# Kernel tuning notes

Measured on AMD Instinct MI355X. Metric: run time of the kernel, lower is better.

## Reference

```python
import jax, jax.numpy as jnp
import numpy as np

N_NODES = 50000


def _graphconv(h, W, b, src, dst, norm_src, norm_dst, activation):
    # DGL GraphConv, norm='both': scale by out-degree^{-1/2} on src side,
    # aggregate (copy_u + sum), scale by in-degree^{-1/2} on dst side.
    in_f, out_f = W.shape
    h = h * norm_src[:, None]
    if in_f > out_f:
        # mult W first to reduce message size (matches DGL branch)
        h = h @ W
        h = jax.ops.segment_sum(h[src], dst, num_segments=N_NODES)
    else:
        h = jax.ops.segment_sum(h[src], dst, num_segments=N_NODES)
        h = h @ W
    h = h * norm_dst[:, None] + b
    if activation:
        h = jax.nn.relu(h)
    return h


def setup_inputs() -> dict:
    key = jax.random.key(0)
    ks = jax.random.split(key, 10)
    N, E = N_NODES, 800000
    in_feats, n_hidden, n_classes = 256, 128, 64
    features = jax.random.normal(ks[0], (N, in_feats), dtype=jnp.float32)
    src = jax.random.randint(ks[1], (E,), 0, N, dtype=jnp.int32)
    dst = jax.random.randint(ks[2], (E,), 0, N, dtype=jnp.int32)
    def glorot(k, shape):
        lim = float(np.sqrt(6.0 / (shape[0] + shape[1])))
        return jax.random.uniform(k, shape, jnp.float32, -lim, lim)
    return {
        "features": features,
        "W1": glorot(ks[3], (in_feats, n_hidden)), "b1": jnp.zeros((n_hidden,), jnp.float32),
        "W2": glorot(ks[4], (n_hidden, n_hidden)), "b2": jnp.zeros((n_hidden,), jnp.float32),
        "W3": glorot(ks[5], (n_hidden, n_classes)), "b3": jnp.zeros((n_classes,), jnp.float32),
        "src": src, "dst": dst,
    }


def reference(features, W1, b1, W2, b2, W3, b3, src, dst):
    ones = jnp.ones(src.shape, jnp.float32)
    deg_out = jax.ops.segment_sum(ones, src, num_segments=N_NODES)
    deg_in = jax.ops.segment_sum(ones, dst, num_segments=N_NODES)
    norm_src = jax.lax.rsqrt(jnp.maximum(deg_out, 1.0))
    norm_dst = jax.lax.rsqrt(jnp.maximum(deg_in, 1.0))
    h = features
    # dropout in eval mode (identity) for deterministic baseline
    h = _graphconv(h, W1, b1, src, dst, norm_src, norm_dst, activation=True)
    h = _graphconv(h, W2, b2, src, dst, norm_src, norm_dst, activation=True)
    h = _graphconv(h, W3, b3, src, dst, norm_src, norm_dst, activation=False)
    return h
```

## Files before the change

### kernel.cpp

```cpp
#include <hip/hip_runtime.h>
#include <math.h>


typedef _Float16 half8 __attribute__((ext_vector_type(8)));
typedef float floatx4 __attribute__((ext_vector_type(4)));

#define TILE 1024
#define BCAP 8192
#define PKW  64
#define EPT  4

__global__ __launch_bounds__(256) void bin_edges(
    const int* __restrict__ src, const int* __restrict__ dst, int E, int NB,
    int* __restrict__ gcurD, int* __restrict__ gcurS,
    ushort2* __restrict__ binD, unsigned short* __restrict__ binS)
{
    __shared__ int lcntD[256], loffD[256], curD[256], lbaseD[256];
    __shared__ int lcntS[256], loffS[256], curS[256], lbaseS[256];
    __shared__ int wtot[4];
    __shared__ ushort2 stageD[TILE];
    __shared__ unsigned short stageS[TILE];

    const int tid = threadIdx.x, lane = tid & 63, wave = tid >> 6;
    const int tile0 = blockIdx.x * TILE;
    const int tn = min(TILE, E - tile0);

    lcntD[tid] = 0;
    lcntS[tid] = 0;
    __syncthreads();

    unsigned short es[EPT], ed[EPT];
    unsigned char ebD[EPT], ebS[EPT];
    int nl = 0;
    for (int i = tid; i < tn; i += 256) {
        int s = src[tile0 + i], d = dst[tile0 + i];
        es[nl] = (unsigned short)s; ed[nl] = (unsigned short)d;
        ebD[nl] = (unsigned char)(d >> 8);
        ebS[nl] = (unsigned char)(s >> 8);
        nl++;
        atomicAdd(&lcntD[d >> 8], 1);
        atomicAdd(&lcntS[s >> 8], 1);
    }
    __syncthreads();

    {
        int v = lcntD[tid], x = v;
#pragma unroll
        for (int o = 1; o < 64; o <<= 1) {
            int t = __shfl_up(x, o, 64);
            if (lane >= o) x += t;
        }
        if (lane == 63) wtot[wave] = x;
        __syncthreads();
        if (tid == 0) {
            int a = 0;
#pragma unroll
            for (int w = 0; w < 4; w++) { int t = wtot[w]; wtot[w] = a; a += t; }
        }
        __syncthreads();
        int excl = x - v + wtot[wave];
        loffD[tid] = excl;
        curD[tid]  = excl;
    }
    __syncthreads();
    {
        int v = lcntS[tid], x = v;
#pragma unroll
        for (int o = 1; o < 64; o <<= 1) {
            int t = __shfl_up(x, o, 64);
            if (lane >= o) x += t;
        }
        if (lane == 63) wtot[wave] = x;
        __syncthreads();
        if (tid == 0) {
            int a = 0;
#pragma unroll
            for (int w = 0; w < 4; w++) { int t = wtot[w]; wtot[w] = a; a += t; }
        }
        __syncthreads();
        int excl = x - v + wtot[wave];
        loffS[tid] = excl;
        curS[tid]  = excl;
    }
    __syncthreads();

    for (int j = 0; j < nl; j++) {
        int pD = atomicAdd(&curD[ebD[j]], 1);
        ushort2 u; u.x = es[j]; u.y = ed[j];
        stageD[pD] = u;
        int pS = atomicAdd(&curS[ebS[j]], 1);
        stageS[pS] = es[j];
    }
    if (tid < NB) {
        if (lcntD[tid] > 0) lbaseD[tid] = atomicAdd(&gcurD[tid], lcntD[tid]);
        if (lcntS[tid] > 0) lbaseS[tid] = atomicAdd(&gcurS[tid], lcntS[tid]);
    }
    __syncthreads();

    for (int i = tid; i < tn; i += 256) {
        {
            int lo = 0, hi = NB - 1;
            while (lo < hi) {
                int mid = (lo + hi + 1) >> 1;
                if (loffD[mid] <= i) lo = mid; else hi = mid - 1;
            }
            int gi = lbaseD[lo] + (i - loffD[lo]);
            if (gi < BCAP)
                binD[(size_t)lo * BCAP + gi] = stageD[i];
        }
        {
            int lo = 0, hi = NB - 1;
            while (lo < hi) {
                int mid = (lo + hi + 1) >> 1;
                if (loffS[mid] <= i) lo = mid; else hi = mid - 1;
            }
            int gi = lbaseS[lo] + (i - loffS[lo]);
            if (gi < BCAP)
                binS[(size_t)lo * BCAP + gi] = stageS[i];
        }
    }
}

__global__ __launch_bounds__(256) void lists_counts(
    const ushort2* __restrict__ binD, const int* __restrict__ gcurD,
    const unsigned short* __restrict__ binS, const int* __restrict__ gcurS,
    unsigned short* __restrict__ packed, int* __restrict__ cntI,
    int* __restrict__ cntO, int N, unsigned short padv)
{
    __shared__ unsigned short stage[256 * PKW];
    __shared__ int lcnt[256];
    __shared__ int h[256];
    const int tid = threadIdx.x;
    const int b = blockIdx.x;
    const int node0 = b << 8;

    lcnt[tid] = 0;
    h[tid] = 0;
    for (int i = tid; i < 256 * PKW; i += 256)
        stage[i] = padv;
    __syncthreads();

    const int nD = min(gcurD[b], BCAP);
    const ushort2* ebD = binD + (size_t)b * BCAP;
    for (int i = tid; i < nD; i += 256) {
        ushort2 e = ebD[i];
        int ld = (int)e.y - node0;
        int p = atomicAdd(&lcnt[ld], 1);
        if (p < PKW) stage[ld * PKW + p] = e.x;
    }
    const int nS = min(gcurS[b], BCAP);
    const unsigned short* ebS = binS + (size_t)b * BCAP;
    for (int i = tid; i < nS; i += 256)
        atomicAdd(&h[(int)ebS[i] - node0], 1);
    __syncthreads();

    int node = node0 + tid;
    if (node < N) {
        cntI[node] = min(lcnt[tid], PKW);
        cntO[node] = h[tid];
    }
    const int wave = tid >> 6, lane = tid & 63;
    for (int ld = wave; ld < 256; ld += 4) {
        int nd = node0 + ld;
        if (nd < N)
            packed[(size_t)nd * PKW + lane] = stage[ld * PKW + lane];
    }
}

__global__ __launch_bounds__(256) void wprep(
    const float* __restrict__ W1, const float* __restrict__ W2,
    const float* __restrict__ W3, _Float16* __restrict__ WT1,
    _Float16* __restrict__ WT2, _Float16* __restrict__ WT3,
    int* __restrict__ gcur, _Float16* __restrict__ z0,
    _Float16* __restrict__ z1)
{
    int i = blockIdx.x * 256 + threadIdx.x;
    if (i < 512) gcur[i] = 0;
    else if (i < 640) z0[i - 512] = (_Float16)0.f;
    else if (i < 768) z1[i - 640] = (_Float16)0.f;
    if (i < 256 * 128) {
        int k = i / 128, n = i - k * 128;
        WT1[(size_t)n * 256 + k] = (_Float16)W1[i];
    } else if (i < 256 * 128 + 128 * 128) {
        int r = i - 256 * 128;
        int k = r / 128, n = r - k * 128;
        WT2[(size_t)n * 128 + k] = (_Float16)W2[r];
    } else if (i < 256 * 128 + 128 * 128 + 128 * 64) {
        int r = i - 256 * 128 - 128 * 128;
        int k = r / 64, n = r - k * 64;
        WT3[(size_t)n * 128 + k] = (_Float16)W3[r];
    }
}

template<int K, int NC, bool A_FP32>
__global__ __launch_bounds__(256) void gemm_mfma(
    const void* __restrict__ A_, const _Float16* __restrict__ WT,
    const int* __restrict__ cnt_rs,
    const int* __restrict__ cnt_nd, const float* __restrict__ bias,
    int do_relu, const int* __restrict__ cnt_ns,
    _Float16* __restrict__ C, int M)
{
    constexpr int NT  = NC / 16;
    constexpr int KC  = 128;
    constexpr int LDW = KC + 8;
    __shared__ _Float16 Bs[NC * LDW];

    const int tid  = threadIdx.x;
    const int wave = tid >> 6;
    const int lane = tid & 63;
    const int quad = lane >> 4;
    const int l16  = lane & 15;

    const int row_base = blockIdx.x * 128 + wave * 32;
    const int ar0 = min(row_base + l16, M - 1);
    const int ar1 = min(row_base + 16 + l16, M - 1);

    floatx4 acc[2][NT];
#pragma unroll
    for (int m = 0; m < 2; m++)
#pragma unroll
        for (int t = 0; t < NT; t++)
            acc[m][t] = (floatx4){0.f, 0.f, 0.f, 0.f};

    float rs0 = 1.0f, rs1 = 1.0f;
    if (A_FP32 && cnt_rs) {
        rs0 = rsqrtf(fmaxf((float)cnt_rs[ar0], 1.0f));
        rs1 = rsqrtf(fmaxf((float)cnt_rs[ar1], 1.0f));
    }

    const float*    Af = (const float*)A_;
    const _Float16* Ah = (const _Float16*)A_;

    for (int kc = 0; kc < K; kc += KC) {
#pragma unroll
        for (int s = tid; s < NC * (KC / 8); s += 256) {
            int row  = s >> 4;
            int col8 = s & 15;
            half8 v = *(const half8*)&WT[(size_t)row * K + kc + col8 * 8];
            *(half8*)&Bs[row * LDW + col8 * 8] = v;
        }
        __syncthreads();
#pragma unroll
        for (int k0 = 0; k0 < KC; k0 += 32) {
            half8 a0, a1;
            if (A_FP32) {
                const float* p0 = &Af[(size_t)ar0 * K + kc + k0 + quad * 8];
                const float* p1 = &Af[(size_t)ar1 * K + kc + k0 + quad * 8];
                float4 f0 = *(const float4*)p0;
                float4 f1 = *(const float4*)(p0 + 4);
                float4 g0 = *(const float4*)p1;
                float4 g1 = *(const float4*)(p1 + 4);
                a0[0] = (_Float16)(f0.x * rs0); a0[1] = (_Float16)(f0.y * rs0);
                a0[2] = (_Float16)(f0.z * rs0); a0[3] = (_Float16)(f0.w * rs0);
                a0[4] = (_Float16)(f1.x * rs0); a0[5] = (_Float16)(f1.y * rs0);
                a0[6] = (_Float16)(f1.z * rs0); a0[7] = (_Float16)(f1.w * rs0);
                a1[0] = (_Float16)(g0.x * rs1); a1[1] = (_Float16)(g0.y * rs1);
                a1[2] = (_Float16)(g0.z * rs1); a1[3] = (_Float16)(g0.w * rs1);
                a1[4] = (_Float16)(g1.x * rs1); a1[5] = (_Float16)(g1.y * rs1);
                a1[6] = (_Float16)(g1.z * rs1); a1[7] = (_Float16)(g1.w * rs1);
            } else {
                a0 = *(const half8*)&Ah[(size_t)ar0 * K + kc + k0 + quad * 8];
                a1 = *(const half8*)&Ah[(size_t)ar1 * K + kc + k0 + quad * 8];
            }
#pragma unroll
            for (int t = 0; t < NT; t++) {
                half8 b = *(const half8*)&Bs[(t * 16 + l16) * LDW + k0 + quad * 8];
                acc[0][t] = __builtin_amdgcn_mfma_f32_16x16x32_f16(a0, b, acc[0][t], 0, 0, 0);
                acc[1][t] = __builtin_amdgcn_mfma_f32_16x16x32_f16(a1, b, acc[1][t], 0, 0, 0);
            }
        }
        __syncthreads();
    }

#pragma unroll
    for (int m = 0; m < 2; m++) {
#pragma unroll
        for (int t = 0; t < NT; t++) {
            int col = t * 16 + l16;
            float bv = bias ? bias[col] : 0.f;
#pragma unroll
            for (int r = 0; r < 4; r++) {
                int row_o = row_base + m * 16 + quad * 4 + r;
                if (row_o < M) {
                    float v = acc[m][t][r];
                    if (cnt_nd) v *= rsqrtf(fmaxf((float)cnt_nd[row_o], 1.0f));
                    v += bv;
                    if (do_relu) v = fmaxf(v, 0.f);
                    if (cnt_ns) v *= rsqrtf(fmaxf((float)cnt_ns[row_o], 1.0f));
                    C[(size_t)row_o * NC + col] = (_Float16)v;
                }
            }
        }
    }
}

__global__ __launch_bounds__(256) void gather128(
    const _Float16* __restrict__ msg, const int* __restrict__ cntI,
    const int* __restrict__ cntO, const unsigned short* __restrict__ packed,
    const float* __restrict__ bias, int do_relu, int use_nd, int use_ns,
    _Float16* __restrict__ out, int N)
{
    int node = (blockIdx.x * 256 + threadIdx.x) >> 6;
    if (node >= N) return;
    int lane = threadIdx.x & 63;
    int grp = lane >> 4, l16 = lane & 15;

    int len = cntI[node];
    const unsigned short* bl = packed + (size_t)node * PKW;
    const half8* mp = (const half8*)msg;

    float a[8];
#pragma unroll
    for (int h = 0; h < 8; h++) a[h] = 0.f;

    int iters = (len + 31) >> 5;
    if (iters < 1) iters = 1;
    for (int it = 0; it < iters; it++) {
        int j = it * 32 + grp;
        int s0 = bl[j],      s1 = bl[j + 4],  s2 = bl[j + 8],  s3 = bl[j + 12];
        int s4 = bl[j + 16], s5 = bl[j + 20], s6 = bl[j + 24], s7 = bl[j + 28];
        half8 v0 = mp[(size_t)s0 * 16 + l16];
        half8 v1 = mp[(size_t)s1 * 16 + l16];
        half8 v2 = mp[(size_t)s2 * 16 + l16];
        half8 v3 = mp[(size_t)s3 * 16 + l16];
        half8 v4 = mp[(size_t)s4 * 16 + l16];
        half8 v5 = mp[(size_t)s5 * 16 + l16];
        half8 v6 = mp[(size_t)s6 * 16 + l16];
        half8 v7 = mp[(size_t)s7 * 16 + l16];
#pragma unroll
        for (int h = 0; h < 8; h++)
            a[h] += (((float)v0[h] + (float)v1[h]) + ((float)v2[h] + (float)v3[h]))
                  + (((float)v4[h] + (float)v5[h]) + ((float)v6[h] + (float)v7[h]));
    }
#pragma unroll
    for (int h = 0; h < 8; h++) {
        a[h] += __shfl_xor(a[h], 16);
        a[h] += __shfl_xor(a[h], 32);
    }

    if (grp == 0) {
        float sc = use_nd ? rsqrtf(fmaxf((float)len, 1.0f)) : 1.0f;
        float pp = use_ns ? rsqrtf(fmaxf((float)cntO[node], 1.0f)) : 1.0f;
        half8 rv;
#pragma unroll
        for (int h = 0; h < 8; h++) {
            float bv = bias ? bias[l16 * 8 + h] : 0.f;
            float r = a[h] * sc + bv;
            if (do_relu) r = fmaxf(r, 0.f);
            rv[h] = (_Float16)(r * pp);
        }
        ((half8*)out)[(size_t)node * 16 + l16] = rv;
    }
}

__global__ __launch_bounds__(256) void gather64(
    const _Float16* __restrict__ msg, const int* __restrict__ cntI,
    const unsigned short* __restrict__ packed, const float* __restrict__ bias,
    float* __restrict__ out, int N)
{
    int node = (blockIdx.x * 256 + threadIdx.x) >> 6;
    if (node >= N) return;
    int lane = threadIdx.x & 63;
    int grp = lane >> 3, l8 = lane & 7;

    int len = cntI[node];
    const unsigned short* bl = packed + (size_t)node * PKW;
    const half8* mp = (const half8*)msg;

    float a[8];
#pragma unroll
    for (int h = 0; h < 8; h++) a[h] = 0.f;

    int iters = (len + 31) >> 5;
    if (iters < 1) iters = 1;
    for (int it = 0; it < iters; it++) {
        int j = it * 32 + grp;
        int s0 = bl[j], s1 = bl[j + 8], s2 = bl[j + 16], s3 = bl[j + 24];
        half8 v0 = mp[(size_t)s0 * 8 + l8];
        half8 v1 = mp[(size_t)s1 * 8 + l8];
        half8 v2 = mp[(size_t)s2 * 8 + l8];
        half8 v3 = mp[(size_t)s3 * 8 + l8];
#pragma unroll
        for (int h = 0; h < 8; h++)
            a[h] += ((float)v0[h] + (float)v1[h]) + ((float)v2[h] + (float)v3[h]);
    }
#pragma unroll
    for (int h = 0; h < 8; h++) {
        a[h] += __shfl_xor(a[h], 8);
        a[h] += __shfl_xor(a[h], 16);
        a[h] += __shfl_xor(a[h], 32);
    }

    if (grp == 0) {
        float sc = rsqrtf(fmaxf((float)len, 1.0f));
        float4 r0, r1;
        r0.x = a[0] * sc + bias[l8 * 8 + 0];
        r0.y = a[1] * sc + bias[l8 * 8 + 1];
        r0.z = a[2] * sc + bias[l8 * 8 + 2];
        r0.w = a[3] * sc + bias[l8 * 8 + 3];
        r1.x = a[4] * sc + bias[l8 * 8 + 4];
        r1.y = a[5] * sc + bias[l8 * 8 + 5];
        r1.z = a[6] * sc + bias[l8 * 8 + 6];
        r1.w = a[7] * sc + bias[l8 * 8 + 7];
        float4* op = (float4*)&out[(size_t)node * 64 + l8 * 8];
        op[0] = r0;
        op[1] = r1;
    }
}

extern "C" void kernel_launch(void* const* d_in, const int* in_sizes, int n_in,
                              void* d_out, int out_size, void* d_ws, size_t ws_size,
                              hipStream_t stream)
{
    const float* X  = (const float*)d_in[0];
    const float* W1 = (const float*)d_in[1];
    const float* b1 = (const float*)d_in[2];
    const float* W2 = (const float*)d_in[3];
    const float* b2 = (const float*)d_in[4];
    const float* W3 = (const float*)d_in[5];
    const float* b3 = (const float*)d_in[6];
    const int*   src = (const int*)d_in[7];
    const int*   dst = (const int*)d_in[8];

    const int N = in_sizes[0] / 256;
    const int E = in_sizes[7];
    const int NB = (N + 255) >> 8;

    char* base = (char*)d_ws;
    size_t cur = 0;
    auto alloc = [&](size_t bytes) -> void* {
        void* p = base + cur;
        cur += (bytes + 255) & ~(size_t)255;
        return p;
    };
    int* gcur2 = (int*)alloc((size_t)2 * 256 * 4);
    int* gcurD = gcur2;
    int* gcurS = gcur2 + 256;
    ushort2*        binD   = (ushort2*)alloc((size_t)NB * BCAP * 4);
    unsigned short* binS   = (unsigned short*)alloc((size_t)NB * BCAP * 2);
    unsigned short* packed = (unsigned short*)alloc((size_t)N * PKW * 2);
    int* cntO = (int*)alloc((size_t)N * 4);
    int* cntI = (int*)alloc((size_t)N * 4);
    _Float16* Bh0 = (_Float16*)alloc(((size_t)N + 1) * 128 * 2);
    _Float16* Bh1 = (_Float16*)alloc(((size_t)N + 1) * 128 * 2);
    _Float16* WT1 = (_Float16*)alloc((size_t)256 * 128 * 2);
    _Float16* WT2 = (_Float16*)alloc((size_t)128 * 128 * 2);
    _Float16* WT3 = (_Float16*)alloc((size_t)128 * 64 * 2);

    const int tblk = (E + TILE - 1) / TILE;
    const int gblk = (N + 127) / 128;
    const int wblk = (N + 3) / 4;

    wprep<<<(256*128 + 128*128 + 128*64 + 255) / 256, 256, 0, stream>>>(
        W1, W2, W3, WT1, WT2, WT3,
        gcur2, Bh0 + (size_t)N * 128, Bh1 + (size_t)N * 128);
    bin_edges<<<tblk, 256, 0, stream>>>(src, dst, E, NB, gcurD, gcurS, binD, binS);
    lists_counts<<<NB, 256, 0, stream>>>(binD, gcurD, binS, gcurS,
                                         packed, cntI, cntO, N,
                                         (unsigned short)N);

    gemm_mfma<256, 128, true><<<gblk, 256, 0, stream>>>(
        X, WT1, cntO, nullptr, nullptr, 0, nullptr, Bh0, N);
    gather128<<<wblk, 256, 0, stream>>>(
        Bh0, cntI, cntO, packed, b1, 1, 1, 1, Bh1, N);

    gather128<<<wblk, 256, 0, stream>>>(
        Bh1, cntI, cntO, packed, nullptr, 0, 0, 0, Bh0, N);
    gemm_mfma<128, 128, false><<<gblk, 256, 0, stream>>>(
        Bh0, WT2, nullptr, cntI, b2, 1, cntO, Bh1, N);

    gemm_mfma<128, 64, false><<<(N + 1 + 127) / 128, 256, 0, stream>>>(
        Bh1, WT3, nullptr, nullptr, nullptr, 0, nullptr, Bh0, N + 1);
    gather64<<<wblk, 256, 0, stream>>>(
        Bh0, cntI, packed, b3, (float*)d_out, N);
}
```

Before: 303.7 us.

## Fuse all GCN stages into one persistent cooperative kernel with grid syncs

Replaces the nine separate kernel launches (weight prep, edge binning, list building, three GEMMs, three gathers) with a single cooperative persistent kernel. Each former kernel becomes a phase with grid-stride loops, and grid-wide barriers separate the phases. The aim is to remove launch overhead and the idle gaps between kernels. In exchange, occupancy is capped by the largest shared-memory and register footprint across all phases, and each phase now runs on a fixed grid instead of its natural launch size.

New measurement: 837.9 us. 176% more time.

```diff
diff --git a/kernel.cpp b/kernel.cpp
--- a/kernel.cpp
+++ b/kernel.cpp
@@ -1,5 +1,8 @@
 #include <hip/hip_runtime.h>
+#include <hip/hip_cooperative_groups.h>
 #include <math.h>
+
+namespace cg = cooperative_groups;
 
 
 typedef _Float16 half8 __attribute__((ext_vector_type(8)));
@@ -9,201 +12,37 @@
 #define BCAP 8192
 #define PKW  64
 #define EPT  4
-
-__global__ __launch_bounds__(256) void bin_edges(
-    const int* __restrict__ src, const int* __restrict__ dst, int E, int NB,
-    int* __restrict__ gcurD, int* __restrict__ gcurS,
-    ushort2* __restrict__ binD, unsigned short* __restrict__ binS)
-{
-    __shared__ int lcntD[256], loffD[256], curD[256], lbaseD[256];
-    __shared__ int lcntS[256], loffS[256], curS[256], lbaseS[256];
-    __shared__ int wtot[4];
-    __shared__ ushort2 stageD[TILE];
-    __shared__ unsigned short stageS[TILE];
-
-    const int tid = threadIdx.x, lane = tid & 63, wave = tid >> 6;
-    const int tile0 = blockIdx.x * TILE;
-    const int tn = min(TILE, E - tile0);
-
-    lcntD[tid] = 0;
-    lcntS[tid] = 0;
-    __syncthreads();
-
-    unsigned short es[EPT], ed[EPT];
-    unsigned char ebD[EPT], ebS[EPT];
-    int nl = 0;
-    for (int i = tid; i < tn; i += 256) {
-        int s = src[tile0 + i], d = dst[tile0 + i];
-        es[nl] = (unsigned short)s; ed[nl] = (unsigned short)d;
-        ebD[nl] = (unsigned char)(d >> 8);
-        ebS[nl] = (unsigned char)(s >> 8);
-        nl++;
-        atomicAdd(&lcntD[d >> 8], 1);
-        atomicAdd(&lcntS[s >> 8], 1);
-    }
-    __syncthreads();
-
-    {
-        int v = lcntD[tid], x = v;
-#pragma unroll
-        for (int o = 1; o < 64; o <<= 1) {
-            int t = __shfl_up(x, o, 64);
-            if (lane >= o) x += t;
-        }
-        if (lane == 63) wtot[wave] = x;
-        __syncthreads();
-        if (tid == 0) {
-            int a = 0;
-#pragma unroll
-            for (int w = 0; w < 4; w++) { int t = wtot[w]; wtot[w] = a; a += t; }
-        }
-        __syncthreads();
-        int excl = x - v + wtot[wave];
-        loffD[tid] = excl;
-        curD[tid]  = excl;
-    }
-    __syncthreads();
-    {
-        int v = lcntS[tid], x = v;
-#pragma unroll
-        for (int o = 1; o < 64; o <<= 1) {
-            int t = __shfl_up(x, o, 64);
-            if (lane >= o) x += t;
-        }
-        if (lane == 63) wtot[wave] = x;
-        __syncthreads();
-        if (tid == 0) {
-            int a = 0;
-#pragma unroll
-            for (int w = 0; w < 4; w++) { int t = wtot[w]; wtot[w] = a; a += t; }
-        }
-        __syncthreads();
-        int excl = x - v + wtot[wave];
-        loffS[tid] = excl;
-        curS[tid]  = excl;
-    }
-    __syncthreads();
-
-    for (int j = 0; j < nl; j++) {
-        int pD = atomicAdd(&curD[ebD[j]], 1);
-        ushort2 u; u.x = es[j]; u.y = ed[j];
-        stageD[pD] = u;
-        int pS = atomicAdd(&curS[ebS[j]], 1);
-        stageS[pS] = es[j];
-    }
-    if (tid < NB) {
-        if (lcntD[tid] > 0) lbaseD[tid] = atomicAdd(&gcurD[tid], lcntD[tid]);
-        if (lcntS[tid] > 0) lbaseS[tid] = atomicAdd(&gcurS[tid], lcntS[tid]);
-    }
-    __syncthreads();
-
-    for (int i = tid; i < tn; i += 256) {
-        {
-            int lo = 0, hi = NB - 1;
-            while (lo < hi) {
-                int mid = (lo + hi + 1) >> 1;
-                if (loffD[mid] <= i) lo = mid; else hi = mid - 1;
-            }
-            int gi = lbaseD[lo] + (i - loffD[lo]);
-            if (gi < BCAP)
-                binD[(size_t)lo * BCAP + gi] = stageD[i];
-        }
-        {
-            int lo = 0, hi = NB - 1;
-            while (lo < hi) {
-                int mid = (lo + hi + 1) >> 1;
-                if (loffS[mid] <= i) lo = mid; else hi = mid - 1;
-            }
-            int gi = lbaseS[lo] + (i - loffS[lo]);
-            if (gi < BCAP)
-                binS[(size_t)lo * BCAP + gi] = stageS[i];
-        }
-    }
-}
-
-__global__ __launch_bounds__(256) void lists_counts(
-    const ushort2* __restrict__ binD, const int* __restrict__ gcurD,
-    const unsigned short* __restrict__ binS, const int* __restrict__ gcurS,
-    unsigned short* __restrict__ packed, int* __restrict__ cntI,
-    int* __restrict__ cntO, int N, unsigned short padv)
-{
-    __shared__ unsigned short stage[256 * PKW];
-    __shared__ int lcnt[256];
-    __shared__ int h[256];
-    const int tid = threadIdx.x;
-    const int b = blockIdx.x;
-    const int node0 = b << 8;
-
-    lcnt[tid] = 0;
-    h[tid] = 0;
-    for (int i = tid; i < 256 * PKW; i += 256)
-        stage[i] = padv;
-    __syncthreads();
-
-    const int nD = min(gcurD[b], BCAP);
-    const ushort2* ebD = binD + (size_t)b * BCAP;
-    for (int i = tid; i < nD; i += 256) {
-        ushort2 e = ebD[i];
-        int ld = (int)e.y - node0;
-        int p = atomicAdd(&lcnt[ld], 1);
-        if (p < PKW) stage[ld * PKW + p] = e.x;
-    }
-    const int nS = min(gcurS[b], BCAP);
-    const unsigned short* ebS = binS + (size_t)b * BCAP;
-    for (int i = tid; i < nS; i += 256)
-        atomicAdd(&h[(int)ebS[i] - node0], 1);
-    __syncthreads();
-
-    int node = node0 + tid;
-    if (node < N) {
-        cntI[node] = min(lcnt[tid], PKW);
-        cntO[node] = h[tid];
-    }
-    const int wave = tid >> 6, lane = tid & 63;
-    for (int ld = wave; ld < 256; ld += 4) {
-        int nd = node0 + ld;
-        if (nd < N)
-            packed[(size_t)nd * PKW + lane] = stage[ld * PKW + lane];
-    }
-}
-
-__global__ __launch_bounds__(256) void wprep(
-    const float* __restrict__ W1, const float* __restrict__ W2,
-    const float* __restrict__ W3, _Float16* __restrict__ WT1,
-    _Float16* __restrict__ WT2, _Float16* __restrict__ WT3,
-    int* __restrict__ gcur, _Float16* __restrict__ z0,
-    _Float16* __restrict__ z1)
-{
-    int i = blockIdx.x * 256 + threadIdx.x;
-    if (i < 512) gcur[i] = 0;
-    else if (i < 640) z0[i - 512] = (_Float16)0.f;
-    else if (i < 768) z1[i - 640] = (_Float16)0.f;
-    if (i < 256 * 128) {
-        int k = i / 128, n = i - k * 128;
-        WT1[(size_t)n * 256 + k] = (_Float16)W1[i];
-    } else if (i < 256 * 128 + 128 * 128) {
-        int r = i - 256 * 128;
-        int k = r / 128, n = r - k * 128;
-        WT2[(size_t)n * 128 + k] = (_Float16)W2[r];
-    } else if (i < 256 * 128 + 128 * 128 + 128 * 64) {
-        int r = i - 256 * 128 - 128 * 128;
-        int k = r / 64, n = r - k * 64;
-        WT3[(size_t)n * 128 + k] = (_Float16)W3[r];
-    }
-}
+#define SMEM_BYTES 35072
+
+struct Params {
+    const float* X;
+    const float* W1; const float* b1;
+    const float* W2; const float* b2;
+    const float* W3; const float* b3;
+    const int* src; const int* dst;
+    int* gcur;
+    ushort2* binD;
+    unsigned short* binS;
+    unsigned short* packed;
+    int* cntO; int* cntI;
+    _Float16* Bh0; _Float16* Bh1;
+    _Float16* WT1; _Float16* WT2; _Float16* WT3;
+    float* out;
+    int N, E, NB, tblk;
+};
 
 template<int K, int NC, bool A_FP32>
-__global__ __launch_bounds__(256) void gemm_mfma(
-    const void* __restrict__ A_, const _Float16* __restrict__ WT,
-    const int* __restrict__ cnt_rs,
-    const int* __restrict__ cnt_nd, const float* __restrict__ bias,
-    int do_relu, const int* __restrict__ cnt_ns,
-    _Float16* __restrict__ C, int M)
+__device__ __forceinline__ void gemm_phase(
+    char* smem_, const void* A_, const _Float16* __restrict__ WT,
+    const int* __restrict__ cnt_rs, const int* __restrict__ cnt_nd,
+    const float* __restrict__ bias, int do_relu,
+    const int* __restrict__ cnt_ns, _Float16* __restrict__ C,
+    int M, int nblocks)
 {
     constexpr int NT  = NC / 16;
     constexpr int KC  = 128;
     constexpr int LDW = KC + 8;
-    __shared__ _Float16 Bs[NC * LDW];
+    _Float16* Bs = (_Float16*)smem_;
 
     const int tid  = threadIdx.x;
     const int wave = tid >> 6;
@@ -211,217 +50,432 @@
     const int quad = lane >> 4;
     const int l16  = lane & 15;
 
-    const int row_base = blockIdx.x * 128 + wave * 32;
-    const int ar0 = min(row_base + l16, M - 1);
-    const int ar1 = min(row_base + 16 + l16, M - 1);
-
-    floatx4 acc[2][NT];
-#pragma unroll
-    for (int m = 0; m < 2; m++)
-#pragma unroll
-        for (int t = 0; t < NT; t++)
-            acc[m][t] = (floatx4){0.f, 0.f, 0.f, 0.f};
-
-    float rs0 = 1.0f, rs1 = 1.0f;
-    if (A_FP32 && cnt_rs) {
-        rs0 = rsqrtf(fmaxf((float)cnt_rs[ar0], 1.0f));
-        rs1 = rsqrtf(fmaxf((float)cnt_rs[ar1], 1.0f));
-    }
-
     const float*    Af = (const float*)A_;
     const _Float16* Ah = (const _Float16*)A_;
-
-    for (int kc = 0; kc < K; kc += KC) {
-#pragma unroll
-        for (int s = tid; s < NC * (KC / 8); s += 256) {
-            int row  = s >> 4;
-            int col8 = s & 15;
-            half8 v = *(const half8*)&WT[(size_t)row * K + kc + col8 * 8];
-            *(half8*)&Bs[row * LDW + col8 * 8] = v;
-        }
-        __syncthreads();
-#pragma unroll
-        for (int k0 = 0; k0 < KC; k0 += 32) {
-            half8 a0, a1;
-            if (A_FP32) {
-                const float* p0 = &Af[(size_t)ar0 * K + kc + k0 + quad * 8];
-                const float* p1 = &Af[(size_t)ar1 * K + kc + k0 + quad * 8];
-                float4 f0 = *(const float4*)p0;
-                float4 f1 = *(const float4*)(p0 + 4);
-                float4 g0 = *(const float4*)p1;
-                float4 g1 = *(const float4*)(p1 + 4);
-                a0[0] = (_Float16)(f0.x * rs0); a0[1] = (_Float16)(f0.y * rs0);
-                a0[2] = (_Float16)(f0.z * rs0); a0[3] = (_Float16)(f0.w * rs0);
-                a0[4] = (_Float16)(f1.x * rs0); a0[5] = (_Float16)(f1.y * rs0);
-                a0[6] = (_Float16)(f1.z * rs0); a0[7] = (_Float16)(f1.w * rs0);
-                a1[0] = (_Float16)(g0.x * rs1); a1[1] = (_Float16)(g0.y * rs1);
-                a1[2] = (_Float16)(g0.z * rs1); a1[3] = (_Float16)(g0.w * rs1);
-                a1[4] = (_Float16)(g1.x * rs1); a1[5] = (_Float16)(g1.y * rs1);
-                a1[6] = (_Float16)(g1.z * rs1); a1[7] = (_Float16)(g1.w * rs1);
-            } else {
-                a0 = *(const half8*)&Ah[(size_t)ar0 * K + kc + k0 + quad * 8];
-                a1 = *(const half8*)&Ah[(size_t)ar1 * K + kc + k0 + quad * 8];
-            }
+    const int gblk = (M + 127) / 128;
+
+    for (int mb = blockIdx.x; mb < gblk; mb += nblocks) {
+        const int row_base = mb * 128 + wave * 32;
+        const int ar0 = min(row_base + l16, M - 1);
+        const int ar1 = min(row_base + 16 + l16, M - 1);
+
+        floatx4 acc[2][NT];
+#pragma unroll
+        for (int m = 0; m < 2; m++)
+#pragma unroll
+            for (int t = 0; t < NT; t++)
+                acc[m][t] = (floatx4){0.f, 0.f, 0.f, 0.f};
+
+        float rs0 = 1.0f, rs1 = 1.0f;
+        if (A_FP32 && cnt_rs) {
+            rs0 = rsqrtf(fmaxf((float)cnt_rs[ar0], 1.0f));
+            rs1 = rsqrtf(fmaxf((float)cnt_rs[ar1], 1.0f));
+        }
+
+        for (int kc = 0; kc < K; kc += KC) {
+#pragma unroll
+            for (int s = tid; s < NC * (KC / 8); s += 256) {
+                int row  = s >> 4;
+                int col8 = s & 15;
+                half8 v = *(const half8*)&WT[(size_t)row * K + kc + col8 * 8];
+                *(half8*)&Bs[row * LDW + col8 * 8] = v;
+            }
+            __syncthreads();
+#pragma unroll
+            for (int k0 = 0; k0 < KC; k0 += 32) {
+                half8 a0, a1;
+                if (A_FP32) {
+                    const float* p0 = &Af[(size_t)ar0 * K + kc + k0 + quad * 8];
+                    const float* p1 = &Af[(size_t)ar1 * K + kc + k0 + quad * 8];
+                    float4 f0 = *(const float4*)p0;
+                    float4 f1 = *(const float4*)(p0 + 4);
+                    float4 g0 = *(const float4*)p1;
+                    float4 g1 = *(const float4*)(p1 + 4);
+                    a0[0] = (_Float16)(f0.x * rs0); a0[1] = (_Float16)(f0.y * rs0);
+                    a0[2] = (_Float16)(f0.z * rs0); a0[3] = (_Float16)(f0.w * rs0);
+                    a0[4] = (_Float16)(f1.x * rs0); a0[5] = (_Float16)(f1.y * rs0);
+                    a0[6] = (_Float16)(f1.z * rs0); a0[7] = (_Float16)(f1.w * rs0);
+                    a1[0] = (_Float16)(g0.x * rs1); a1[1] = (_Float16)(g0.y * rs1);
+                    a1[2] = (_Float16)(g0.z * rs1); a1[3] = (_Float16)(g0.w * rs1);
+                    a1[4] = (_Float16)(g1.x * rs1); a1[5] = (_Float16)(g1.y * rs1);
+                    a1[6] = (_Float16)(g1.z * rs1); a1[7] = (_Float16)(g1.w * rs1);
+                } else {
+                    a0 = *(const half8*)&Ah[(size_t)ar0 * K + kc + k0 + quad * 8];
+                    a1 = *(const half8*)&Ah[(size_t)ar1 * K + kc + k0 + quad * 8];
+                }
+#pragma unroll
+                for (int t = 0; t < NT; t++) {
+                    half8 b = *(const half8*)&Bs[(t * 16 + l16) * LDW + k0 + quad * 8];
+                    acc[0][t] = __builtin_amdgcn_mfma_f32_16x16x32_f16(a0, b, acc[0][t], 0, 0, 0);
+                    acc[1][t] = __builtin_amdgcn_mfma_f32_16x16x32_f16(a1, b, acc[1][t], 0, 0, 0);
+                }
+            }
+            __syncthreads();
+        }
+
+#pragma unroll
+        for (int m = 0; m < 2; m++) {
 #pragma unroll
             for (int t = 0; t < NT; t++) {
-                half8 b = *(const half8*)&Bs[(t * 16 + l16) * LDW + k0 + quad * 8];
-                acc[0][t] = __builtin_amdgcn_mfma_f32_16x16x32_f16(a0, b, acc[0][t], 0, 0, 0);
-                acc[1][t] = __builtin_amdgcn_mfma_f32_16x16x32_f16(a1, b, acc[1][t], 0, 0, 0);
-            }
-        }
-        __syncthreads();
-    }
-
-#pragma unroll
-    for (int m = 0; m < 2; m++) {
-#pragma unroll
-        for (int t = 0; t < NT; t++) {
-            int col = t * 16 + l16;
-            float bv = bias ? bias[col] : 0.f;
-#pragma unroll
-            for (int r = 0; r < 4; r++) {
-                int row_o = row_base + m * 16 + quad * 4 + r;
-                if (row_o < M) {
-                    float v = acc[m][t][r];
-                    if (cnt_nd) v *= rsqrtf(fmaxf((float)cnt_nd[row_o], 1.0f));
-                    v += bv;
-                    if (do_relu) v = fmaxf(v, 0.f);
-                    if (cnt_ns) v *= rsqrtf(fmaxf((float)cnt_ns[row_o], 1.0f));
-                    C[(size_t)row_o * NC + col] = (_Float16)v;
+                int col = t * 16 + l16;
+                float bv = bias ? bias[col] : 0.f;
+#pragma unroll
+                for (int r = 0; r < 4; r++) {
+                    int row_o = row_base + m * 16 + quad * 4 + r;
+                    if (row_o < M) {
+                        float v = acc[m][t][r];
+                        if (cnt_nd) v *= rsqrtf(fmaxf((float)cnt_nd[row_o], 1.0f));
+                        v += bv;
+                        if (do_relu) v = fmaxf(v, 0.f);
+                        if (cnt_ns) v *= rsqrtf(fmaxf((float)cnt_ns[row_o], 1.0f));
+                        C[(size_t)row_o * NC + col] = (_Float16)v;
+                    }
                 }
             }
         }
     }
 }
 
-__global__ __launch_bounds__(256) void gather128(
+__device__ __forceinline__ void gather128_phase(
     const _Float16* __restrict__ msg, const int* __restrict__ cntI,
     const int* __restrict__ cntO, const unsigned short* __restrict__ packed,
     const float* __restrict__ bias, int do_relu, int use_nd, int use_ns,
-    _Float16* __restrict__ out, int N)
+    _Float16* __restrict__ out, int N, int gwave, int nwaves)
 {
-    int node = (blockIdx.x * 256 + threadIdx.x) >> 6;
-    if (node >= N) return;
     int lane = threadIdx.x & 63;
     int grp = lane >> 4, l16 = lane & 15;
-
-    int len = cntI[node];
-    const unsigned short* bl = packed + (size_t)node * PKW;
     const half8* mp = (const half8*)msg;
 
-    float a[8];
-#pragma unroll
-    for (int h = 0; h < 8; h++) a[h] = 0.f;
-
-    int iters = (len + 31) >> 5;
-    if (iters < 1) iters = 1;
-    for (int it = 0; it < iters; it++) {
-        int j = it * 32 + grp;
-        int s0 = bl[j],      s1 = bl[j + 4],  s2 = bl[j + 8],  s3 = bl[j + 12];
-        int s4 = bl[j + 16], s5 = bl[j + 20], s6 = bl[j + 24], s7 = bl[j + 28];
-        half8 v0 = mp[(size_t)s0 * 16 + l16];
-        half8 v1 = mp[(size_t)s1 * 16 + l16];
-        half8 v2 = mp[(size_t)s2 * 16 + l16];
-        half8 v3 = mp[(size_t)s3 * 16 + l16];
-        half8 v4 = mp[(size_t)s4 * 16 + l16];
-        half8 v5 = mp[(size_t)s5 * 16 + l16];
-        half8 v6 = mp[(size_t)s6 * 16 + l16];
-        half8 v7 = mp[(size_t)s7 * 16 + l16];
-#pragma unroll
-        for (int h = 0; h < 8; h++)
-            a[h] += (((float)v0[h] + (float)v1[h]) + ((float)v2[h] + (float)v3[h]))
-                  + (((float)v4[h] + (float)v5[h]) + ((float)v6[h] + (float)v7[h]));
-    }
-#pragma unroll
-    for (int h = 0; h < 8; h++) {
-        a[h] += __shfl_xor(a[h], 16);
-        a[h] += __shfl_xor(a[h], 32);
-    }
-
-    if (grp == 0) {
-        float sc = use_nd ? rsqrtf(fmaxf((float)len, 1.0f)) : 1.0f;
-        float pp = use_ns ? rsqrtf(fmaxf((float)cntO[node], 1.0f)) : 1.0f;
-        half8 rv;
+    for (int node = gwave; node < N; node += nwaves) {
+        int len = cntI[node];
+        const unsigned short* bl = packed + (size_t)node * PKW;
+
+        float a[8];
+#pragma unroll
+        for (int h = 0; h < 8; h++) a[h] = 0.f;
+
+        int iters = (len + 31) >> 5;
+        if (iters < 1) iters = 1;
+        for (int it = 0; it < iters; it++) {
+            int j = it * 32 + grp;
+            int s0 = bl[j],      s1 = bl[j + 4],  s2 = bl[j + 8],  s3 = bl[j + 12];
+            int s4 = bl[j + 16], s5 = bl[j + 20], s6 = bl[j + 24], s7 = bl[j + 28];
+            half8 v0 = mp[(size_t)s0 * 16 + l16];
+            half8 v1 = mp[(size_t)s1 * 16 + l16];
+            half8 v2 = mp[(size_t)s2 * 16 + l16];
+            half8 v3 = mp[(size_t)s3 * 16 + l16];
+            half8 v4 = mp[(size_t)s4 * 16 + l16];
+            half8 v5 = mp[(size_t)s5 * 16 + l16];
+            half8 v6 = mp[(size_t)s6 * 16 + l16];
+            half8 v7 = mp[(size_t)s7 * 16 + l16];
+#pragma unroll
+            for (int h = 0; h < 8; h++)
+                a[h] += (((float)v0[h] + (float)v1[h]) + ((float)v2[h] + (float)v3[h]))
+                      + (((float)v4[h] + (float)v5[h]) + ((float)v6[h] + (float)v7[h]));
+        }
 #pragma unroll
         for (int h = 0; h < 8; h++) {
-            float bv = bias ? bias[l16 * 8 + h] : 0.f;
-            float r = a[h] * sc + bv;
-            if (do_relu) r = fmaxf(r, 0.f);
-            rv[h] = (_Float16)(r * pp);
-        }
-        ((half8*)out)[(size_t)node * 16 + l16] = rv;
+            a[h] += __shfl_xor(a[h], 16);
+            a[h] += __shfl_xor(a[h], 32);
+        }
+
+        if (grp == 0) {
+            float sc = use_nd ? rsqrtf(fmaxf((float)len, 1.0f)) : 1.0f;
+            float pp = use_ns ? rsqrtf(fmaxf((float)cntO[node], 1.0f)) : 1.0f;
+            half8 rv;
+#pragma unroll
+            for (int h = 0; h < 8; h++) {
+                float bv = bias ? bias[l16 * 8 + h] : 0.f;
+                float r = a[h] * sc + bv;
+                if (do_relu) r = fmaxf(r, 0.f);
+                rv[h] = (_Float16)(r * pp);
+            }
+            ((half8*)out)[(size_t)node * 16 + l16] = rv;
+        }
     }
 }
 
-__global__ __launch_bounds__(256) void gather64(
+__device__ __forceinline__ void gather64_phase(
     const _Float16* __restrict__ msg, const int* __restrict__ cntI,
     const unsigned short* __restrict__ packed, const float* __restrict__ bias,
-    float* __restrict__ out, int N)
+    float* __restrict__ out, int N, int gwave, int nwaves)
 {
-    int node = (blockIdx.x * 256 + threadIdx.x) >> 6;
-    if (node >= N) return;
     int lane = threadIdx.x & 63;
     int grp = lane >> 3, l8 = lane & 7;
-
-    int len = cntI[node];
-    const unsigned short* bl = packed + (size_t)node * PKW;
     const half8* mp = (const half8*)msg;
 
-    float a[8];
-#pragma unroll
-    for (int h = 0; h < 8; h++) a[h] = 0.f;
-
-    int iters = (len + 31) >> 5;
-    if (iters < 1) iters = 1;
-    for (int it = 0; it < iters; it++) {
-        int j = it * 32 + grp;
-        int s0 = bl[j], s1 = bl[j + 8], s2 = bl[j + 16], s3 = bl[j + 24];
-        half8 v0 = mp[(size_t)s0 * 8 + l8];
-        half8 v1 = mp[(size_t)s1 * 8 + l8];
-        half8 v2 = mp[(size_t)s2 * 8 + l8];
-        half8 v3 = mp[(size_t)s3 * 8 + l8];
-#pragma unroll
-        for (int h = 0; h < 8; h++)
-            a[h] += ((float)v0[h] + (float)v1[h]) + ((float)v2[h] + (float)v3[h]);
+    for (int node = gwave; node < N; node += nwaves) {
+        int len = cntI[node];
+        const unsigned short* bl = packed + (size_t)node * PKW;
+
+        float a[8];
+#pragma unroll
+        for (int h = 0; h < 8; h++) a[h] = 0.f;
+
+        int iters = (len + 31) >> 5;
+        if (iters < 1) iters = 1;
+        for (int it = 0; it < iters; it++) {
+            int j = it * 32 + grp;
+            int s0 = bl[j], s1 = bl[j + 8], s2 = bl[j + 16], s3 = bl[j + 24];
+            half8 v0 = mp[(size_t)s0 * 8 + l8];
+            half8 v1 = mp[(size_t)s1 * 8 + l8];
+            half8 v2 = mp[(size_t)s2 * 8 + l8];
+            half8 v3 = mp[(size_t)s3 * 8 + l8];
+#pragma unroll
+            for (int h = 0; h < 8; h++)
+                a[h] += ((float)v0[h] + (float)v1[h]) + ((float)v2[h] + (float)v3[h]);
+        }
+#pragma unroll
+        for (int h = 0; h < 8; h++) {
+            a[h] += __shfl_xor(a[h], 8);
+            a[h] += __shfl_xor(a[h], 16);
+            a[h] += __shfl_xor(a[h], 32);
+        }
+
+        if (grp == 0) {
+            float sc = rsqrtf(fmaxf((float)len, 1.0f));
+            float4 r0, r1;
+            r0.x = a[0] * sc + bias[l8 * 8 + 0];
+            r0.y = a[1] * sc + bias[l8 * 8 + 1];
+            r0.z = a[2] * sc + bias[l8 * 8 + 2];
+            r0.w = a[3] * sc + bias[l8 * 8 + 3];
+            r1.x = a[4] * sc + bias[l8 * 8 + 4];
+            r1.y = a[5] * sc + bias[l8 * 8 + 5];
+            r1.z = a[6] * sc + bias[l8 * 8 + 6];
+            r1.w = a[7] * sc + bias[l8 * 8 + 7];
+            float4* op = (float4*)&out[(size_t)node * 64 + l8 * 8];
+            op[0] = r0;
+            op[1] = r1;
+        }
     }
-#pragma unroll
-    for (int h = 0; h < 8; h++) {
-        a[h] += __shfl_xor(a[h], 8);
-        a[h] += __shfl_xor(a[h], 16);
-        a[h] += __shfl_xor(a[h], 32);
+}
+
+__global__ __launch_bounds__(256, 4) void mega(Params p)
+{
+    cg::grid_group gg = cg::this_grid();
+    __shared__ __align__(16) char smem[SMEM_BYTES];
+
+    const int tid = threadIdx.x;
+    const int lane = tid & 63;
+    const int wave = tid >> 6;
+    const int nblocks = gridDim.x;
+    const int nthreads = nblocks * 256;
+    const int gwave = blockIdx.x * 4 + wave;
+    const int nwaves = nblocks * 4;
+
+    {
+        const int TT = 256 * 128 + 128 * 128 + 128 * 64;
+        for (int i = blockIdx.x * 256 + tid; i < TT; i += nthreads) {
+            if (i < 256 * 128) {
+                int k = i / 128, n = i - k * 128;
+                p.WT1[(size_t)n * 256 + k] = (_Float16)p.W1[i];
+            } else if (i < 256 * 128 + 128 * 128) {
+                int r = i - 256 * 128;
+                int k = r / 128, n = r - k * 128;
+                p.WT2[(size_t)n * 128 + k] = (_Float16)p.W2[r];
+            } else {
+                int r = i - 256 * 128 - 128 * 128;
+                int k = r / 64, n = r - k * 64;
+                p.WT3[(size_t)n * 128 + k] = (_Float16)p.W3[r];
+            }
+        }
+        int i = blockIdx.x * 256 + tid;
+        if (i < 512) p.gcur[i] = 0;
+        else if (i < 640) p.Bh0[(size_t)p.N * 128 + (i - 512)] = (_Float16)0.f;
+        else if (i < 768) p.Bh1[(size_t)p.N * 128 + (i - 640)] = (_Float16)0.f;
     }
-
-    if (grp == 0) {
-        float sc = rsqrtf(fmaxf((float)len, 1.0f));
-        float4 r0, r1;
-        r0.x = a[0] * sc + bias[l8 * 8 + 0];
-        r0.y = a[1] * sc + bias[l8 * 8 + 1];
-        r0.z = a[2] * sc + bias[l8 * 8 + 2];
-        r0.w = a[3] * sc + bias[l8 * 8 + 3];
-        r1.x = a[4] * sc + bias[l8 * 8 + 4];
-        r1.y = a[5] * sc + bias[l8 * 8 + 5];
-        r1.z = a[6] * sc + bias[l8 * 8 + 6];
-        r1.w = a[7] * sc + bias[l8 * 8 + 7];
-        float4* op = (float4*)&out[(size_t)node * 64 + l8 * 8];
-        op[0] = r0;
-        op[1] = r1;
+    gg.sync();
+
+    {
+        int* lcntD  = (int*)smem;
+        int* loffD  = lcntD + 256;
+        int* curD   = loffD + 256;
+        int* lbaseD = curD + 256;
+        int* lcntS  = lbaseD + 256;
+        int* loffS  = lcntS + 256;
+        int* curS   = loffS + 256;
+        int* lbaseS = curS + 256;
+        int* wtot   = lbaseS + 256;
+        ushort2* stageD = (ushort2*)(smem + 8208);
+        unsigned short* stageS = (unsigned short*)(smem + 12304);
+        int* gcurD = p.gcur;
+        int* gcurS = p.gcur + 256;
+
+        for (int tile = blockIdx.x; tile < p.tblk; tile += nblocks) {
+            const int tile0 = tile * TILE;
+            const int tn = min(TILE, p.E - tile0);
+
+            lcntD[tid] = 0;
+            lcntS[tid] = 0;
+            __syncthreads();
+
+            unsigned short es[EPT], ed[EPT];
+            unsigned char ebD[EPT], ebS[EPT];
+            int nl = 0;
+            for (int i = tid; i < tn; i += 256) {
+                int s = p.src[tile0 + i], d = p.dst[tile0 + i];
+                es[nl] = (unsigned short)s; ed[nl] = (unsigned short)d;
+                ebD[nl] = (unsigned char)(d >> 8);
+                ebS[nl] = (unsigned char)(s >> 8);
+                nl++;
+                atomicAdd(&lcntD[d >> 8], 1);
+                atomicAdd(&lcntS[s >> 8], 1);
+            }
+            __syncthreads();
+
+            {
+                int v = lcntD[tid], x = v;
+#pragma unroll
+                for (int o = 1; o < 64; o <<= 1) {
+                    int t = __shfl_up(x, o, 64);
+                    if (lane >= o) x += t;
+                }
+                if (lane == 63) wtot[wave] = x;
+                __syncthreads();
+                if (tid == 0) {
+                    int a = 0;
+#pragma unroll
+                    for (int w = 0; w < 4; w++) { int t = wtot[w]; wtot[w] = a; a += t; }
+                }
+                __syncthreads();
+                int excl = x - v + wtot[wave];
+                loffD[tid] = excl;
+                curD[tid]  = excl;
+            }
+            __syncthreads();
+            {
+                int v = lcntS[tid], x = v;
+#pragma unroll
+                for (int o = 1; o < 64; o <<= 1) {
+                    int t = __shfl_up(x, o, 64);
+                    if (lane >= o) x += t;
+                }
+                if (lane == 63) wtot[wave] = x;
+                __syncthreads();
+                if (tid == 0) {
+                    int a = 0;
+#pragma unroll
+                    for (int w = 0; w < 4; w++) { int t = wtot[w]; wtot[w] = a; a += t; }
+                }
+                __syncthreads();
+                int excl = x - v + wtot[wave];
+                loffS[tid] = excl;
+                curS[tid]  = excl;
+            }
+            __syncthreads();
+
+            for (int j = 0; j < nl; j++) {
+                int pD = atomicAdd(&curD[ebD[j]], 1);
+                ushort2 u; u.x = es[j]; u.y = ed[j];
+                stageD[pD] = u;
+                int pS = atomicAdd(&curS[ebS[j]], 1);
+                stageS[pS] = es[j];
+            }
+            if (tid < p.NB) {
+                if (lcntD[tid] > 0) lbaseD[tid] = atomicAdd(&gcurD[tid], lcntD[tid]);
+                if (lcntS[tid] > 0) lbaseS[tid] = atomicAdd(&gcurS[tid], lcntS[tid]);
+            }
+            __syncthreads();
+
+            for (int i = tid; i < tn; i += 256) {
+                {
+                    int lo = 0, hi = p.NB - 1;
+                    while (lo < hi) {
+                        int mid = (lo + hi + 1) >> 1;
+                        if (loffD[mid] <= i) lo = mid; else hi = mid - 1;
+                    }
+                    int gi = lbaseD[lo] + (i - loffD[lo]);
+                    if (gi < BCAP)
+                        p.binD[(size_t)lo * BCAP + gi] = stageD[i];
+                }
+                {
+                    int lo = 0, hi = p.NB - 1;
+                    while (lo < hi) {
+                        int mid = (lo + hi + 1) >> 1;
+                        if (loffS[mid] <= i) lo = mid; else hi = mid - 1;
+                    }
+                    int gi = lbaseS[lo] + (i - loffS[lo]);
+                    if (gi < BCAP)
+                        p.binS[(size_t)lo * BCAP + gi] = stageS[i];
+                }
+            }
+            __syncthreads();
+        }
     }
+    gg.sync();
+
+    {
+        int* lcnt = (int*)smem;
+        int* h    = lcnt + 256;
+        unsigned short* stage = (unsigned short*)(smem + 2048);
+        int* gcurD = p.gcur;
+        int* gcurS = p.gcur + 256;
+        unsigned short padv = (unsigned short)p.N;
+
+        for (int b = blockIdx.x; b < p.NB; b += nblocks) {
+            __syncthreads();
+            const int node0 = b << 8;
+            lcnt[tid] = 0;
+            h[tid] = 0;
+            for (int i = tid; i < 256 * PKW; i += 256)
+                stage[i] = padv;
+            __syncthreads();
+
+            const int nD = min(gcurD[b], BCAP);
+            const ushort2* ebD = p.binD + (size_t)b * BCAP;
+            for (int i = tid; i < nD; i += 256) {
+                ushort2 e = ebD[i];
+                int ld = (int)e.y - node0;
+                int q = atomicAdd(&lcnt[ld], 1);
+                if (q < PKW) stage[ld * PKW + q] = e.x;
+            }
+            const int nS = min(gcurS[b], BCAP);
+            const unsigned short* ebS = p.binS + (size_t)b * BCAP;
+            for (int i = tid; i < nS; i += 256)
+                atomicAdd(&h[(int)ebS[i] - node0], 1);
+            __syncthreads();
+
+            int node = node0 + tid;
+            if (node < p.N) {
+                p.cntI[node] = min(lcnt[tid], PKW);
+                p.cntO[node] = h[tid];
+            }
+            for (int ld = wave; ld < 256; ld += 4) {
+                int nd = node0 + ld;
+                if (nd < p.N)
+                    p.packed[(size_t)nd * PKW + lane] = stage[ld * PKW + lane];
+            }
+        }
+    }
+    gg.sync();
+
+    gemm_phase<256, 128, true>(smem, p.X, p.WT1, p.cntO,
+                               nullptr, nullptr, 0, nullptr, p.Bh0, p.N, nblocks);
+    gg.sync();
+
+    gather128_phase(p.Bh0, p.cntI, p.cntO, p.packed, p.b1, 1, 1, 1,
+                    p.Bh1, p.N, gwave, nwaves);
+    gg.sync();
+
+    gather128_phase(p.Bh1, p.cntI, p.cntO, p.packed, nullptr, 0, 0, 0,
+                    p.Bh0, p.N, gwave, nwaves);
+    gg.sync();
+
+    gemm_phase<128, 128, false>(smem, p.Bh0, p.WT2, nullptr,
+                                p.cntI, p.b2, 1, p.cntO, p.Bh1, p.N, nblocks);
+    gg.sync();
+
+    gemm_phase<128, 64, false>(smem, p.Bh1, p.WT3, nullptr,
+                               nullptr, nullptr, 0, nullptr, p.Bh0, p.N + 1, nblocks);
+    gg.sync();
+
+    gather64_phase(p.Bh0, p.cntI, p.packed, p.b3, p.out, p.N, gwave, nwaves);
 }
 
 extern "C" void kernel_launch(void* const* d_in, const int* in_sizes, int n_in,
                               void* d_out, int out_size, void* d_ws, size_t ws_size,
                               hipStream_t stream)
 {
-    const float* X  = (const float*)d_in[0];
-    const float* W1 = (const float*)d_in[1];
-    const float* b1 = (const float*)d_in[2];
-    const float* W2 = (const float*)d_in[3];
-    const float* b2 = (const float*)d_in[4];
-    const float* W3 = (const float*)d_in[5];
-    const float* b3 = (const float*)d_in[6];
-    const int*   src = (const int*)d_in[7];
-    const int*   dst = (const int*)d_in[8];
-
     const int N = in_sizes[0] / 256;
     const int E = in_sizes[7];
     const int NB = (N + 255) >> 8;
@@ -433,44 +487,38 @@
         cur += (bytes + 255) & ~(size_t)255;
         return p;
     };
-    int* gcur2 = (int*)alloc((size_t)2 * 256 * 4);
-    int* gcurD = gcur2;
-    int* gcurS = gcur2 + 256;
-    ushort2*        binD   = (ushort2*)alloc((size_t)NB * BCAP * 4);
-    unsigned short* binS   = (unsigned short*)alloc((size_t)NB * BCAP * 2);
-    unsigned short* packed = (unsigned short*)alloc((size_t)N * PKW * 2);
-    int* cntO = (int*)alloc((size_t)N * 4);
-    int* cntI = (int*)alloc((size_t)N * 4);
-    _Float16* Bh0 = (_Float16*)alloc(((size_t)N + 1) * 128 * 2);
-    _Float16* Bh1 = (_Float16*)alloc(((size_t)N + 1) * 128 * 2);
-    _Float16* WT1 = (_Float16*)alloc((size_t)256 * 128 * 2);
-    _Float16* WT2 = (_Float16*)alloc((size_t)128 * 128 * 2);
-    _Float16* WT3 = (_Float16*)alloc((size_t)128 * 64 * 2);
-
-    const int tblk = (E + TILE - 1) / TILE;
-    const int gblk = (N + 127) / 128;
-    const int wblk = (N + 3) / 4;
-
-    wprep<<<(256*128 + 128*128 + 128*64 + 255) / 256, 256, 0, stream>>>(
-        W1, W2, W3, WT1, WT2, WT3,
-        gcur2, Bh0 + (size_t)N * 128, Bh1 + (size_t)N * 128);
-    bin_edges<<<tblk, 256, 0, stream>>>(src, dst, E, NB, gcurD, gcurS, binD, binS);
-    lists_counts<<<NB, 256, 0, stream>>>(binD, gcurD, binS, gcurS,
-                                         packed, cntI, cntO, N,
-                                         (unsigned short)N);
-
-    gemm_mfma<256, 128, true><<<gblk, 256, 0, stream>>>(
-        X, WT1, cntO, nullptr, nullptr, 0, nullptr, Bh0, N);
-    gather128<<<wblk, 256, 0, stream>>>(
-        Bh0, cntI, cntO, packed, b1, 1, 1, 1, Bh1, N);
-
-    gather128<<<wblk, 256, 0, stream>>>(
-        Bh1, cntI, cntO, packed, nullptr, 0, 0, 0, Bh0, N);
-    gemm_mfma<128, 128, false><<<gblk, 256, 0, stream>>>(
-        Bh0, WT2, nullptr, cntI, b2, 1, cntO, Bh1, N);
-
-    gemm_mfma<128, 64, false><<<(N + 1 + 127) / 128, 256, 0, stream>>>(
-        Bh1, WT3, nullptr, nullptr, nullptr, 0, nullptr, Bh0, N + 1);
-    gather64<<<wblk, 256, 0, stream>>>(
-        Bh0, cntI, packed, b3, (float*)d_out, N);
+
+    Params p;
+    p.X  = (const float*)d_in[0];
+    p.W1 = (const float*)d_in[1]; p.b1 = (const float*)d_in[2];
+    p.W2 = (const float*)d_in[3]; p.b2 = (const float*)d_in[4];
+    p.W3 = (const float*)d_in[5]; p.b3 = (const float*)d_in[6];
+    p.src = (const int*)d_in[7];
+    p.dst = (const int*)d_in[8];
+    p.gcur   = (int*)alloc((size_t)512 * 4);
+    p.binD   = (ushort2*)alloc((size_t)NB * BCAP * 4);
+    p.binS   = (unsigned short*)alloc((size_t)NB * BCAP * 2);
+    p.packed = (unsigned short*)alloc((size_t)N * PKW * 2);
+    p.cntO   = (int*)alloc((size_t)N * 4);
+    p.cntI   = (int*)alloc((size_t)N * 4);
+    p.Bh0    = (_Float16*)alloc(((size_t)N + 1) * 128 * 2);
+    p.Bh1    = (_Float16*)alloc(((size_t)N + 1) * 128 * 2);
+    p.WT1    = (_Float16*)alloc((size_t)256 * 128 * 2);
+    p.WT2    = (_Float16*)alloc((size_t)128 * 128 * 2);
+    p.WT3    = (_Float16*)alloc((size_t)128 * 64 * 2);
+    p.out    = (float*)d_out;
+    p.N = N; p.E = E; p.NB = NB;
+    p.tblk = (E + TILE - 1) / TILE;
+
+    int maxb = 0;
+    if (hipOccupancyMaxActiveBlocksPerMultiprocessor(&maxb, (const void*)mega,
+                                                     256, 0) != hipSuccess ||
+        maxb < 1)
+        maxb = 2;
+    int grid = maxb * 256;
+    if (grid > 2048) grid = 2048;
+
+    void* args[] = { (void*)&p };
+    hipLaunchCooperativeKernel((void*)mega, dim3(grid), dim3(256),
+                               args, 0, stream);
 }
```
